# Kernel tuning notes

Hardware: AMD Instinct MI355X
Metric: run time of the kernel (lower is better)

The kernel has to match this reference:

```python
import jax, jax.numpy as jnp
import numpy as np

# Synthetic NEAT-style layered DAG (matches init_kwargs)
N_IN = 512      # input nodes
L = 5           # computed layers (last = outputs)
M = 2048        # nodes per computed layer
FAN = 32        # incoming edges per computed node
B = 1024        # batch size
N = N_IN + L * M        # total nodes
E = M * FAN             # edges per layer (grouped by destination layer)


def setup_inputs() -> dict:
    rng = np.random.default_rng(0)
    src = np.zeros((L, E), np.int32)
    dst = np.zeros((L, E), np.int32)
    for l in range(L):
        prefix = N_IN + l * M  # edges may come from any earlier node (DAG w/ skips)
        src[l] = rng.integers(0, prefix, size=E)
        dst[l] = np.repeat(np.arange(M, dtype=np.int32), FAN)
    key = jax.random.key(0)
    k1, k2, k3 = jax.random.split(key, 3)
    x = jax.random.normal(k1, (B, N_IN), jnp.float32)
    weights = jax.random.normal(k2, (L, E), jnp.float32) * 0.1
    biases = jax.random.normal(k3, (L, M), jnp.float32) * 0.01
    return {
        "x": x,
        "weights": weights,
        "biases": biases,
        "src_idx": jnp.asarray(src),
        "dst_idx": jnp.asarray(dst),
    }


def reference(x, weights, biases, src_idx, dst_idx):
    b = x.shape[0]
    # values[:, node] as in the torch module; inputs copied in first
    vals = jnp.zeros((b, N), x.dtype).at[:, :N_IN].set(x)
    for l in range(L):  # topological layers (fixed, small count)
        # gather source activations for this layer's edges and weight them
        contrib = vals[:, src_idx[l]] * weights[l]                    # [B, E]
        # scatter-add into destination nodes of this layer
        layer = jnp.zeros((b, M), x.dtype).at[:, dst_idx[l]].add(contrib)
        layer = jax.nn.relu(layer + biases[l])
        vals = vals.at[:, N_IN + l * M : N_IN + (l + 1) * M].set(layer)
    # output nodes = last computed layer
    return vals[:, N_IN + (L - 1) * M :]
```

## Files before the change

### kernel.cpp

```cpp
#include <hip/hip_runtime.h>

#define N_IN    512
#define NLAYERS 5
#define M_NODES 2048
#define FAN     32
#define B_BATCH 1024
#define E_EDGES (M_NODES * FAN)
#define N_TOTAL (N_IN + NLAYERS * M_NODES)
#define PREFIX4 (N_IN + 4 * M_NODES)

#define CB      4
#define NBLK    (B_BATCH / CB)
#define GROUPS  (M_NODES / 64)
#define ECH     (FAN / 4)

typedef unsigned short u16;
typedef unsigned int   u32;

__device__ __forceinline__ u32 f2bf15_hi(float f) {
    u32 b = __float_as_uint(f);
    return (b + 0xFFFFu + ((b >> 17) & 1u)) & 0xFFFE0000u;
}

typedef __fp16 h2 __attribute__((ext_vector_type(2)));
__device__ __forceinline__ u32 pk_f16(float a, float b) {
    h2 r = __builtin_amdgcn_cvt_pkrtz(a, b);
    u32 u;
    __builtin_memcpy(&u, &r, 4);
    return u;
}

__global__ __launch_bounds__(1024) void pack_edges(
    const float* __restrict__ w,
    const int* __restrict__ src,
    u32* __restrict__ pck) {
    __shared__ u32 s_sorted[64][32];
    __shared__ int s_cnt[64][16];
    __shared__ int s_start[64][16];

    const int t  = threadIdx.x;
    const int lg = blockIdx.x;
    const size_t ebase = (size_t)lg * 2048;

    if (t < 64 * 16) ((int*)s_cnt)[t] = 0;
    __syncthreads();

    const int e0 = t * 2;
    const int node = e0 >> 5;
    const int2   s2 = *reinterpret_cast<const int2*>(src + ebase + e0);
    const float2 w2 = *reinterpret_cast<const float2*>(w + ebase + e0);
    const u32 wd0 = f2bf15_hi(w2.x) | ((u32)s2.x << 3);
    const u32 wd1 = f2bf15_hi(w2.y) | ((u32)s2.y << 3);
    atomicAdd(&s_cnt[node][s2.x & 15], 1);
    atomicAdd(&s_cnt[node][s2.y & 15], 1);
    __syncthreads();

    if (t < 64) {
        int acc = 0;
#pragma unroll
        for (int i = 0; i < 16; ++i) {
            s_start[t][i] = acc;
            acc += s_cnt[t][i];
        }
    }
    __syncthreads();

    const int rot = node & 31;
    {
        const int r0 = atomicAdd(&s_start[node][(wd0 >> 3) & 15], 1);
        s_sorted[node][(r0 + rot) & 31] = wd0;
        const int r1 = atomicAdd(&s_start[node][(wd1 >> 3) & 15], 1);
        s_sorted[node][(r1 + rot) & 31] = wd1;
    }
    __syncthreads();

#pragma unroll
    for (int i = 0; i < 2; ++i) {
        const int p    = t + i * 1024;
        const int lane = (p >> 2) & 63;
        const int kp   = ((p >> 8) << 2) | (p & 3);
        pck[ebase + p] = s_sorted[lane][kp];
    }
}

__global__ __launch_bounds__(1024) void net_kernel(
    const float* __restrict__ x,
    const u32* __restrict__ pck,
    const float* __restrict__ bias,
    float* __restrict__ out) {
    __shared__ uint2 vals2[PREFIX4];

    const int t   = threadIdx.x;
    const int blk = blockIdx.x;

    if (t < N_IN) {
        const float v0 = x[(size_t)(CB * blk + 0) * N_IN + t];
        const float v1 = x[(size_t)(CB * blk + 1) * N_IN + t];
        const float v2 = x[(size_t)(CB * blk + 2) * N_IN + t];
        const float v3 = x[(size_t)(CB * blk + 3) * N_IN + t];
        vals2[t] = make_uint2(pk_f16(v0, v1), pk_f16(v2, v3));
    }

    const int g0    = t >> 6;
    const int lane6 = t & 63;
    const char* vbase = reinterpret_cast<const char*>(vals2);

    for (int l = 0; l < NLAYERS; ++l) {
        __syncthreads();
        const int base = N_IN + l * M_NODES;
#pragma unroll
        for (int r = 0; r < 2; ++r) {
            const int j = r * 1024 + t;
            const uint4* ep = reinterpret_cast<const uint4*>(pck) +
                              (size_t)(l * GROUPS + g0 + r * 16) * ECH * 64 +
                              lane6;
            const float bj = bias[l * M_NODES + j];
            float a0 = bj, a1 = bj, a2 = bj, a3 = bj;

            uint4 wd = ep[0];
#pragma unroll
            for (int ec = 0; ec < ECH; ++ec) {
                const uint4 nxt = (ec < ECH - 1) ? ep[(ec + 1) * 64] : wd;
                const u32 ew[4] = {wd.x, wd.y, wd.z, wd.w};
                uint2 v[4];
#pragma unroll
                for (int c = 0; c < 4; ++c)
                    v[c] = *reinterpret_cast<const uint2*>(
                        vbase + (ew[c] & 0x1FFF8u));
#pragma unroll
                for (int c = 0; c < 4; ++c) {
                    const float wv = __uint_as_float(ew[c] & 0xFFFE0000u);
                    asm("v_fma_mix_f32 %0, %1, %2, %0 op_sel:[0,0,0] op_sel_hi:[0,1,0]"
                        : "+v"(a0) : "v"(wv), "v"(v[c].x));
                    asm("v_fma_mix_f32 %0, %1, %2, %0 op_sel:[0,1,0] op_sel_hi:[0,1,0]"
                        : "+v"(a1) : "v"(wv), "v"(v[c].x));
                    asm("v_fma_mix_f32 %0, %1, %2, %0 op_sel:[0,0,0] op_sel_hi:[0,1,0]"
                        : "+v"(a2) : "v"(wv), "v"(v[c].y));
                    asm("v_fma_mix_f32 %0, %1, %2, %0 op_sel:[0,1,0] op_sel_hi:[0,1,0]"
                        : "+v"(a3) : "v"(wv), "v"(v[c].y));
                }
                wd = nxt;
            }
            a0 = fmaxf(a0, 0.f);
            a1 = fmaxf(a1, 0.f);
            a2 = fmaxf(a2, 0.f);
            a3 = fmaxf(a3, 0.f);
            if (l < NLAYERS - 1) {
                vals2[base + j] = make_uint2(pk_f16(a0, a1), pk_f16(a2, a3));
            } else {
                out[(size_t)(CB * blk + 0) * M_NODES + j] = a0;
                out[(size_t)(CB * blk + 1) * M_NODES + j] = a1;
                out[(size_t)(CB * blk + 2) * M_NODES + j] = a2;
                out[(size_t)(CB * blk + 3) * M_NODES + j] = a3;
            }
        }
    }
}

extern "C" void kernel_launch(void* const* d_in, const int* in_sizes, int n_in,
                              void* d_out, int out_size, void* d_ws, size_t ws_size,
                              hipStream_t stream) {
    const float* x       = (const float*)d_in[0];
    const float* weights = (const float*)d_in[1];
    const float* biases  = (const float*)d_in[2];
    const int*   src_idx = (const int*)d_in[3];
    float* out = (float*)d_out;
    u32*   pck = (u32*)d_ws;

    pack_edges<<<NLAYERS * GROUPS, 1024, 0, stream>>>(weights, src_idx, pck);

    net_kernel<<<NBLK, 1024, 0, stream>>>(x, pck, biases, out);
}
```

Measured before the change: 87.66 us.

## Halve per-block batch to two samples for more resident blocks and bank-sorted gathers

Each block now processes two batch rows instead of four, storing activations as one packed f16 pair (4 bytes) per node. This halves the LDS footprint so two blocks can share a CU, and it doubles the grid size. The edge packer now sorts each node's edges by source index modulo 32 rather than 16, to match the new 4-byte stride to LDS banks. In exchange, each edge fetch and LDS gather now serves only two batch rows, so total gather and edge-load instructions roughly double across the grid.

```diff
diff --git a/kernel.cpp b/kernel.cpp
--- a/kernel.cpp
+++ b/kernel.cpp
@@ -9,7 +9,7 @@
 #define N_TOTAL (N_IN + NLAYERS * M_NODES)
 #define PREFIX4 (N_IN + 4 * M_NODES)
 
-#define CB      4
+#define CB      2
 #define NBLK    (B_BATCH / CB)
 #define GROUPS  (M_NODES / 64)
 #define ECH     (FAN / 4)
@@ -35,30 +35,31 @@
     const int* __restrict__ src,
     u32* __restrict__ pck) {
     __shared__ u32 s_sorted[64][32];
-    __shared__ int s_cnt[64][16];
-    __shared__ int s_start[64][16];
+    __shared__ int s_cnt[64][32];
+    __shared__ int s_start[64][32];
 
     const int t  = threadIdx.x;
     const int lg = blockIdx.x;
     const size_t ebase = (size_t)lg * 2048;
 
-    if (t < 64 * 16) ((int*)s_cnt)[t] = 0;
+    ((int*)s_cnt)[t]        = 0;
+    ((int*)s_cnt)[t + 1024] = 0;
     __syncthreads();
 
     const int e0 = t * 2;
     const int node = e0 >> 5;
     const int2   s2 = *reinterpret_cast<const int2*>(src + ebase + e0);
     const float2 w2 = *reinterpret_cast<const float2*>(w + ebase + e0);
-    const u32 wd0 = f2bf15_hi(w2.x) | ((u32)s2.x << 3);
-    const u32 wd1 = f2bf15_hi(w2.y) | ((u32)s2.y << 3);
-    atomicAdd(&s_cnt[node][s2.x & 15], 1);
-    atomicAdd(&s_cnt[node][s2.y & 15], 1);
+    const u32 wd0 = f2bf15_hi(w2.x) | ((u32)s2.x << 2);
+    const u32 wd1 = f2bf15_hi(w2.y) | ((u32)s2.y << 2);
+    atomicAdd(&s_cnt[node][s2.x & 31], 1);
+    atomicAdd(&s_cnt[node][s2.y & 31], 1);
     __syncthreads();
 
     if (t < 64) {
         int acc = 0;
 #pragma unroll
-        for (int i = 0; i < 16; ++i) {
+        for (int i = 0; i < 32; ++i) {
             s_start[t][i] = acc;
             acc += s_cnt[t][i];
         }
@@ -67,9 +68,9 @@
 
     const int rot = node & 31;
     {
-        const int r0 = atomicAdd(&s_start[node][(wd0 >> 3) & 15], 1);
+        const int r0 = atomicAdd(&s_start[node][(wd0 >> 2) & 31], 1);
         s_sorted[node][(r0 + rot) & 31] = wd0;
-        const int r1 = atomicAdd(&s_start[node][(wd1 >> 3) & 15], 1);
+        const int r1 = atomicAdd(&s_start[node][(wd1 >> 2) & 31], 1);
         s_sorted[node][(r1 + rot) & 31] = wd1;
     }
     __syncthreads();
@@ -83,12 +84,12 @@
     }
 }
 
-__global__ __launch_bounds__(1024) void net_kernel(
+__global__ __launch_bounds__(1024, 8) void net_kernel(
     const float* __restrict__ x,
     const u32* __restrict__ pck,
     const float* __restrict__ bias,
     float* __restrict__ out) {
-    __shared__ uint2 vals2[PREFIX4];
+    __shared__ u32 vals[PREFIX4];
 
     const int t   = threadIdx.x;
     const int blk = blockIdx.x;
@@ -96,14 +97,12 @@
     if (t < N_IN) {
         const float v0 = x[(size_t)(CB * blk + 0) * N_IN + t];
         const float v1 = x[(size_t)(CB * blk + 1) * N_IN + t];
-        const float v2 = x[(size_t)(CB * blk + 2) * N_IN + t];
-        const float v3 = x[(size_t)(CB * blk + 3) * N_IN + t];
-        vals2[t] = make_uint2(pk_f16(v0, v1), pk_f16(v2, v3));
+        vals[t] = pk_f16(v0, v1);
     }
 
     const int g0    = t >> 6;
     const int lane6 = t & 63;
-    const char* vbase = reinterpret_cast<const char*>(vals2);
+    const char* vbase = reinterpret_cast<const char*>(vals);
 
     for (int l = 0; l < NLAYERS; ++l) {
         __syncthreads();
@@ -115,43 +114,35 @@
                               (size_t)(l * GROUPS + g0 + r * 16) * ECH * 64 +
                               lane6;
             const float bj = bias[l * M_NODES + j];
-            float a0 = bj, a1 = bj, a2 = bj, a3 = bj;
+            float a0 = bj, a1 = bj;
 
             uint4 wd = ep[0];
 #pragma unroll
             for (int ec = 0; ec < ECH; ++ec) {
                 const uint4 nxt = (ec < ECH - 1) ? ep[(ec + 1) * 64] : wd;
                 const u32 ew[4] = {wd.x, wd.y, wd.z, wd.w};
-                uint2 v[4];
+                u32 v[4];
 #pragma unroll
                 for (int c = 0; c < 4; ++c)
-                    v[c] = *reinterpret_cast<const uint2*>(
-                        vbase + (ew[c] & 0x1FFF8u));
+                    v[c] = *reinterpret_cast<const u32*>(
+                        vbase + (ew[c] & 0xFFFCu));
 #pragma unroll
                 for (int c = 0; c < 4; ++c) {
                     const float wv = __uint_as_float(ew[c] & 0xFFFE0000u);
                     asm("v_fma_mix_f32 %0, %1, %2, %0 op_sel:[0,0,0] op_sel_hi:[0,1,0]"
-                        : "+v"(a0) : "v"(wv), "v"(v[c].x));
+                        : "+v"(a0) : "v"(wv), "v"(v[c]));
                     asm("v_fma_mix_f32 %0, %1, %2, %0 op_sel:[0,1,0] op_sel_hi:[0,1,0]"
-                        : "+v"(a1) : "v"(wv), "v"(v[c].x));
-                    asm("v_fma_mix_f32 %0, %1, %2, %0 op_sel:[0,0,0] op_sel_hi:[0,1,0]"
-                        : "+v"(a2) : "v"(wv), "v"(v[c].y));
-                    asm("v_fma_mix_f32 %0, %1, %2, %0 op_sel:[0,1,0] op_sel_hi:[0,1,0]"
-                        : "+v"(a3) : "v"(wv), "v"(v[c].y));
+                        : "+v"(a1) : "v"(wv), "v"(v[c]));
                 }
                 wd = nxt;
             }
             a0 = fmaxf(a0, 0.f);
             a1 = fmaxf(a1, 0.f);
-            a2 = fmaxf(a2, 0.f);
-            a3 = fmaxf(a3, 0.f);
             if (l < NLAYERS - 1) {
-                vals2[base + j] = make_uint2(pk_f16(a0, a1), pk_f16(a2, a3));
+                vals[base + j] = pk_f16(a0, a1);
             } else {
                 out[(size_t)(CB * blk + 0) * M_NODES + j] = a0;
                 out[(size_t)(CB * blk + 1) * M_NODES + j] = a1;
-                out[(size_t)(CB * blk + 2) * M_NODES + j] = a2;
-                out[(size_t)(CB * blk + 3) * M_NODES + j] = a3;
             }
         }
     }
```

Result: slower. 99.25 us (+13.2%).
